# Kernel optimization log

Measured on AMD Instinct MI355X. Metric: run time of the kernel, lower is better.

## Reference

```python
import jax, jax.numpy as jnp
import numpy as np

B, T, IN_DIM, HIDDEN, OUT_DIM = 256, 4096, 2, 136, 68


def setup_inputs() -> dict:
    key = jax.random.key(0)
    ks = jax.random.split(key, 7)
    s_ih = 1.0 / np.sqrt(HIDDEN)
    return {
        "x": jax.random.normal(ks[0], (B, T, IN_DIM), dtype=jnp.float32),
        "W_ih": jax.random.uniform(ks[1], (HIDDEN, IN_DIM), jnp.float32, -s_ih, s_ih),
        "W_hh": jax.random.uniform(ks[2], (HIDDEN, HIDDEN), jnp.float32, -s_ih, s_ih),
        "b_ih": jax.random.uniform(ks[3], (HIDDEN,), jnp.float32, -s_ih, s_ih),
        "b_hh": jax.random.uniform(ks[4], (HIDDEN,), jnp.float32, -s_ih, s_ih),
        "W_fc": jax.random.uniform(ks[5], (OUT_DIM, HIDDEN), jnp.float32, -s_ih, s_ih),
        "b_fc": jax.random.uniform(ks[6], (OUT_DIM,), jnp.float32, -s_ih, s_ih),
    }


def reference(x, W_ih, W_hh, b_ih, b_hh, W_fc, b_fc):
    # Precompute input projection for all timesteps: [B, T, H]
    xp = jnp.einsum("bti,hi->bth", x, W_ih) + b_ih + b_hh
    h0 = jnp.zeros((x.shape[0], W_hh.shape[0]), dtype=x.dtype)

    def step(h, xp_t):  # h: [B,H], xp_t: [B,H]
        h_new = jnp.tanh(xp_t + h @ W_hh.T)
        return h_new, None

    # scan over time axis (move T to leading axis)
    h_last, _ = jax.lax.scan(step, h0, jnp.swapaxes(xp, 0, 1))
    # final linear head on last hidden state: [B, OUT]
    return h_last @ W_fc.T + b_fc
```

## Files before the change

kernel.cpp:

```cpp
#include <hip/hip_runtime.h>

#define BATCH 256
#define TSTEPS 4096
#define HID 136
#define HPADH 144
#define ODIM 68
#define THREADS 256

typedef _Float16 h2 __attribute__((ext_vector_type(2)));

#define BAR_LDS() asm volatile("s_waitcnt lgkmcnt(0)\n\ts_barrier" ::: "memory")

__device__ __forceinline__ float fast_tanh(float z) {
    float az = fabsf(z);
    float e = __expf(-2.0f * az);
    float r = (1.0f - e) * __builtin_amdgcn_rcpf(1.0f + e);
    return copysignf(r, z);
}

template <int CTRL>
__device__ __forceinline__ float dpp_add(float x) {
    int y = __builtin_amdgcn_update_dpp(0, __float_as_int(x), CTRL, 0xF, 0xF, false);
    return x + __int_as_float(y);
}
__device__ __forceinline__ float reduce8(float x) {
    x = dpp_add<0xB1>(x);
    x = dpp_add<0x4E>(x);
    x = dpp_add<0x141>(x);
    return x;
}

__device__ __forceinline__ h2 bc_h2(unsigned int u) {
    union { unsigned int u; h2 h; } c; c.u = u; return c.h;
}

#define RNN_STEP(HR, HW, XV)                                                   \
    {                                                                          \
        uint4 u0 = *(const uint4*)((HR) + 16 * ks);                            \
        uint4 u1 = *(const uint4*)((HR) + 16 * ks + 8);                        \
        unsigned int ut = *(const unsigned int*)((HR) + 128 + 2 * ks);         \
        h2 hq[9];                                                              \
        hq[0] = bc_h2(u0.x); hq[1] = bc_h2(u0.y);                              \
        hq[2] = bc_h2(u0.z); hq[3] = bc_h2(u0.w);                              \
        hq[4] = bc_h2(u1.x); hq[5] = bc_h2(u1.y);                              \
        hq[6] = bc_h2(u1.z); hq[7] = bc_h2(u1.w);                              \
        hq[8] = bc_h2(ut);                                                     \
        float a0 = 0.f, a1 = 0.f, a2 = 0.f, a3 = 0.f, a4 = 0.f;                \
        _Pragma("unroll")                                                      \
        for (int q = 0; q < 9; ++q) {                                          \
            a0 = __builtin_amdgcn_fdot2(hq[q], wq[0][q], a0, false);           \
            a1 = __builtin_amdgcn_fdot2(hq[q], wq[1][q], a1, false);           \
            a2 = __builtin_amdgcn_fdot2(hq[q], wq[2][q], a2, false);           \
            a3 = __builtin_amdgcn_fdot2(hq[q], wq[3][q], a3, false);           \
            a4 = __builtin_amdgcn_fdot2(hq[q], wq[4][q], a4, false);           \
        }                                                                      \
        a0 = reduce8(a0);                                                      \
        a1 = reduce8(a1);                                                      \
        a2 = reduce8(a2);                                                      \
        a3 = reduce8(a3);                                                      \
        a4 = reduce8(a4);                                                      \
        float s = a0;                                                          \
        s = (ks == 1) ? a1 : s;                                                \
        s = (ks == 2) ? a2 : s;                                                \
        s = (ks == 3) ? a3 : s;                                                \
        s = (ks == 4) ? a4 : s;                                                \
        float z = fmaf((XV).x, wih0, fmaf((XV).y, wih1, bias)) + s;            \
        float th = fast_tanh(z);                                               \
        if (ks < 4 || (ks == 4 && grp < 2)) (HW)[zrow] = (_Float16)th;         \
    }

__global__ __launch_bounds__(THREADS)
void rnn_fused_kernel(const float* __restrict__ x,
                      const float* __restrict__ W_ih,
                      const float* __restrict__ W_hh,
                      const float* __restrict__ b_ih,
                      const float* __restrict__ b_hh,
                      const float* __restrict__ W_fc,
                      const float* __restrict__ b_fc,
                      float* __restrict__ out)
{
    __shared__ __align__(16) _Float16 hA[HPADH];
    __shared__ __align__(16) _Float16 hB[HPADH];

    const int b   = blockIdx.x;
    const int tid = threadIdx.x;
    const int wv  = tid >> 6;
    const int grp = (tid >> 3) & 7;
    const int g   = tid >> 3;
    const int ks  = tid & 7;

    const int erow = 128 + 2 * wv + (g & 1);

    h2 wq[5][9];
#pragma unroll
    for (int j = 0; j < 5; ++j) {
        const int row = (j < 4) ? (4 * g + j) : erow;
#pragma unroll
        for (int q = 0; q < 9; ++q) {
            const int k = (q < 8) ? (16 * ks + 2 * q) : (128 + 2 * ks);
            const float v0 = (k     < HID) ? W_hh[row * HID + k]     : 0.0f;
            const float v1 = (k + 1 < HID) ? W_hh[row * HID + k + 1] : 0.0f;
            wq[j][q] = h2{(_Float16)v0, (_Float16)v1};
        }
    }
    const int zrow = (ks < 4) ? (4 * g + ks) : (ks == 4) ? erow : (4 * g);
    const float wih0 = W_ih[zrow * 2 + 0];
    const float wih1 = W_ih[zrow * 2 + 1];
    const float bias = b_ih[zrow] + b_hh[zrow];

    if (tid < HPADH) { hA[tid] = (_Float16)0.f; hB[tid] = (_Float16)0.f; }
    __syncthreads();

    const float2* xg = (const float2*)(x + (size_t)b * (TSTEPS * 2));
    float2 xc0 = xg[0], xc1 = xg[1];
    float2 xn0 = xg[2], xn1 = xg[3];

    for (int t = 0; t < TSTEPS; t += 2) {
        const int tf = (t + 4) & (TSTEPS - 1);
        const float2 xf0 = xg[tf];
        const float2 xf1 = xg[tf + 1];

        RNN_STEP(hA, hB, xc0);
        BAR_LDS();
        RNN_STEP(hB, hA, xc1);
        BAR_LDS();

        xc0 = xn0; xc1 = xn1;
        xn0 = xf0; xn1 = xf1;
    }

    if (tid < ODIM) {
        const int o = tid;
        float s = b_fc[o];
#pragma unroll 8
        for (int k = 0; k < HID; ++k)
            s = fmaf((float)hA[k], W_fc[o * HID + k], s);
        out[b * ODIM + o] = s;
    }
}

extern "C" void kernel_launch(void* const* d_in, const int* in_sizes, int n_in,
                              void* d_out, int out_size, void* d_ws, size_t ws_size,
                              hipStream_t stream) {
    const float* x    = (const float*)d_in[0];
    const float* W_ih = (const float*)d_in[1];
    const float* W_hh = (const float*)d_in[2];
    const float* b_ih = (const float*)d_in[3];
    const float* b_hh = (const float*)d_in[4];
    const float* W_fc = (const float*)d_in[5];
    const float* b_fc = (const float*)d_in[6];
    float* out = (float*)d_out;

    rnn_fused_kernel<<<BATCH, THREADS, 0, stream>>>(x, W_ih, W_hh, b_ih, b_hh,
                                                    W_fc, b_fc, out);
}
```

Before: 1.149 ms.

## Pack two batch rows per 512-thread block to interleave recurrences

Each block now runs two independent batch recurrences in separate halves of a 512-thread block, with per-half LDS hidden-state buffers, and launches half as many blocks. The intent is to let one CU overlap the latency chains of two sequences. In exchange, only half the CUs are used, and every step synchronizes 8 waves with a full __syncthreads instead of the lighter LDS-only barrier.

```diff
diff --git a/kernel.cpp b/kernel.cpp
--- a/kernel.cpp
+++ b/kernel.cpp
@@ -5,11 +5,10 @@
 #define HID 136
 #define HPADH 144
 #define ODIM 68
-#define THREADS 256
+#define THREADS 512
+#define NBLK (BATCH / 2)
 
 typedef _Float16 h2 __attribute__((ext_vector_type(2)));
-
-#define BAR_LDS() asm volatile("s_waitcnt lgkmcnt(0)\n\ts_barrier" ::: "memory")
 
 __device__ __forceinline__ float fast_tanh(float z) {
     float az = fabsf(z);
@@ -79,17 +78,19 @@
                       const float* __restrict__ b_fc,
                       float* __restrict__ out)
 {
-    __shared__ __align__(16) _Float16 hA[HPADH];
-    __shared__ __align__(16) _Float16 hB[HPADH];
+    __shared__ __align__(16) _Float16 hA[2][HPADH];
+    __shared__ __align__(16) _Float16 hB[2][HPADH];
 
-    const int b   = blockIdx.x;
     const int tid = threadIdx.x;
-    const int wv  = tid >> 6;
-    const int grp = (tid >> 3) & 7;
-    const int g   = tid >> 3;
+    const int sub = tid >> 8;
+    const int st  = tid & 255;
+    const int wvs = st >> 6;
+    const int grp = (st >> 3) & 7;
+    const int g   = st >> 3;
     const int ks  = tid & 7;
+    const int bb  = blockIdx.x * 2 + sub;
 
-    const int erow = 128 + 2 * wv + (g & 1);
+    const int erow = 128 + 2 * wvs + (g & 1);
 
     h2 wq[5][9];
 #pragma unroll
@@ -108,10 +109,13 @@
     const float wih1 = W_ih[zrow * 2 + 1];
     const float bias = b_ih[zrow] + b_hh[zrow];
 
-    if (tid < HPADH) { hA[tid] = (_Float16)0.f; hB[tid] = (_Float16)0.f; }
+    if (st < HPADH) { hA[sub][st] = (_Float16)0.f; hB[sub][st] = (_Float16)0.f; }
     __syncthreads();
 
-    const float2* xg = (const float2*)(x + (size_t)b * (TSTEPS * 2));
+    _Float16* const hAs = hA[sub];
+    _Float16* const hBs = hB[sub];
+
+    const float2* xg = (const float2*)(x + (size_t)bb * (TSTEPS * 2));
     float2 xc0 = xg[0], xc1 = xg[1];
     float2 xn0 = xg[2], xn1 = xg[3];
 
@@ -120,22 +124,22 @@
         const float2 xf0 = xg[tf];
         const float2 xf1 = xg[tf + 1];
 
-        RNN_STEP(hA, hB, xc0);
-        BAR_LDS();
-        RNN_STEP(hB, hA, xc1);
-        BAR_LDS();
+        RNN_STEP(hAs, hBs, xc0);
+        __syncthreads();
+        RNN_STEP(hBs, hAs, xc1);
+        __syncthreads();
 
         xc0 = xn0; xc1 = xn1;
         xn0 = xf0; xn1 = xf1;
     }
 
-    if (tid < ODIM) {
-        const int o = tid;
+    if (st < ODIM) {
+        const int o = st;
         float s = b_fc[o];
 #pragma unroll 8
         for (int k = 0; k < HID; ++k)
-            s = fmaf((float)hA[k], W_fc[o * HID + k], s);
-        out[b * ODIM + o] = s;
+            s = fmaf((float)hAs[k], W_fc[o * HID + k], s);
+        out[bb * ODIM + o] = s;
     }
 }
 
@@ -151,6 +155,6 @@
     const float* b_fc = (const float*)d_in[6];
     float* out = (float*)d_out;
 
-    rnn_fused_kernel<<<BATCH, THREADS, 0, stream>>>(x, W_ih, W_hh, b_ih, b_hh,
-                                                    W_fc, b_fc, out);
+    rnn_fused_kernel<<<NBLK, THREADS, 0, stream>>>(x, W_ih, W_hh, b_ih, b_hh,
+                                                   W_fc, b_fc, out);
 }
```

Result: slower. 1.772 ms (+54.2%).

## Assign one full hidden row per thread, dropping cross-lane DPP reduction

Applied to the files above, without the earlier changes.

Reworks the per-step matvec so each of 192 threads owns one full W_hh row (68 packed half2 weights in registers) and reads the whole hidden vector from LDS as broadcast loads. This removes the 8-lane DPP reduction, the select logic and the redundant row duplication, replacing them with a longer serial dot-product chain per thread. It uses 3 waves instead of 4, raises register pressure to roughly 68+68 VGPRs, and replaces the custom LDS barrier with __syncthreads.

```diff
diff --git a/kernel.cpp b/kernel.cpp
--- a/kernel.cpp
+++ b/kernel.cpp
@@ -3,13 +3,10 @@
 #define BATCH 256
 #define TSTEPS 4096
 #define HID 136
-#define HPADH 144
 #define ODIM 68
-#define THREADS 256
+#define THREADS 192
 
 typedef _Float16 h2 __attribute__((ext_vector_type(2)));
-
-#define BAR_LDS() asm volatile("s_waitcnt lgkmcnt(0)\n\ts_barrier" ::: "memory")
 
 __device__ __forceinline__ float fast_tanh(float z) {
     float az = fabsf(z);
@@ -18,55 +15,27 @@
     return copysignf(r, z);
 }
 
-template <int CTRL>
-__device__ __forceinline__ float dpp_add(float x) {
-    int y = __builtin_amdgcn_update_dpp(0, __float_as_int(x), CTRL, 0xF, 0xF, false);
-    return x + __int_as_float(y);
-}
-__device__ __forceinline__ float reduce8(float x) {
-    x = dpp_add<0xB1>(x);
-    x = dpp_add<0x4E>(x);
-    x = dpp_add<0x141>(x);
-    return x;
-}
-
 __device__ __forceinline__ h2 bc_h2(unsigned int u) {
     union { unsigned int u; h2 h; } c; c.u = u; return c.h;
 }
 
 #define RNN_STEP(HR, HW, XV)                                                   \
     {                                                                          \
-        uint4 u0 = *(const uint4*)((HR) + 16 * ks);                            \
-        uint4 u1 = *(const uint4*)((HR) + 16 * ks + 8);                        \
-        unsigned int ut = *(const unsigned int*)((HR) + 128 + 2 * ks);         \
-        h2 hq[9];                                                              \
-        hq[0] = bc_h2(u0.x); hq[1] = bc_h2(u0.y);                              \
-        hq[2] = bc_h2(u0.z); hq[3] = bc_h2(u0.w);                              \
-        hq[4] = bc_h2(u1.x); hq[5] = bc_h2(u1.y);                              \
-        hq[6] = bc_h2(u1.z); hq[7] = bc_h2(u1.w);                              \
-        hq[8] = bc_h2(ut);                                                     \
-        float a0 = 0.f, a1 = 0.f, a2 = 0.f, a3 = 0.f, a4 = 0.f;                \
+        uint4 hc[17];                                                          \
         _Pragma("unroll")                                                      \
-        for (int q = 0; q < 9; ++q) {                                          \
-            a0 = __builtin_amdgcn_fdot2(hq[q], wq[0][q], a0, false);           \
-            a1 = __builtin_amdgcn_fdot2(hq[q], wq[1][q], a1, false);           \
-            a2 = __builtin_amdgcn_fdot2(hq[q], wq[2][q], a2, false);           \
-            a3 = __builtin_amdgcn_fdot2(hq[q], wq[3][q], a3, false);           \
-            a4 = __builtin_amdgcn_fdot2(hq[q], wq[4][q], a4, false);           \
+        for (int i = 0; i < 17; ++i) hc[i] = ((const uint4*)(HR))[i];          \
+        float a0 = 0.f, a1 = 0.f, a2 = 0.f, a3 = 0.f;                          \
+        _Pragma("unroll")                                                      \
+        for (int i = 0; i < 17; ++i) {                                         \
+            a0 = __builtin_amdgcn_fdot2(bc_h2(hc[i].x), w[4 * i + 0], a0, false); \
+            a1 = __builtin_amdgcn_fdot2(bc_h2(hc[i].y), w[4 * i + 1], a1, false); \
+            a2 = __builtin_amdgcn_fdot2(bc_h2(hc[i].z), w[4 * i + 2], a2, false); \
+            a3 = __builtin_amdgcn_fdot2(bc_h2(hc[i].w), w[4 * i + 3], a3, false); \
         }                                                                      \
-        a0 = reduce8(a0);                                                      \
-        a1 = reduce8(a1);                                                      \
-        a2 = reduce8(a2);                                                      \
-        a3 = reduce8(a3);                                                      \
-        a4 = reduce8(a4);                                                      \
-        float s = a0;                                                          \
-        s = (ks == 1) ? a1 : s;                                                \
-        s = (ks == 2) ? a2 : s;                                                \
-        s = (ks == 3) ? a3 : s;                                                \
-        s = (ks == 4) ? a4 : s;                                                \
-        float z = fmaf((XV).x, wih0, fmaf((XV).y, wih1, bias)) + s;            \
+        float z = (a0 + a1) + (a2 + a3)                                        \
+                + fmaf((XV).x, wih0, fmaf((XV).y, wih1, bias));                \
         float th = fast_tanh(z);                                               \
-        if (ks < 4 || (ks == 4 && grp < 2)) (HW)[zrow] = (_Float16)th;         \
+        if (valid) (HW)[row] = (_Float16)th;                                   \
     }
 
 __global__ __launch_bounds__(THREADS)
@@ -79,36 +48,30 @@
                       const float* __restrict__ b_fc,
                       float* __restrict__ out)
 {
-    __shared__ __align__(16) _Float16 hA[HPADH];
-    __shared__ __align__(16) _Float16 hB[HPADH];
+    __shared__ __align__(16) _Float16 hA[HID];
+    __shared__ __align__(16) _Float16 hB[HID];
 
-    const int b   = blockIdx.x;
-    const int tid = threadIdx.x;
-    const int wv  = tid >> 6;
-    const int grp = (tid >> 3) & 7;
-    const int g   = tid >> 3;
-    const int ks  = tid & 7;
+    const int b     = blockIdx.x;
+    const int tid   = threadIdx.x;
+    const int row   = tid;
+    const bool valid = (row < HID);
+    const int rowc  = valid ? row : 0;
 
-    const int erow = 128 + 2 * wv + (g & 1);
+    h2 w[68];
+#pragma unroll
+    for (int p = 0; p < 68; ++p) {
+        const float v0 = valid ? W_hh[rowc * HID + 2 * p]     : 0.0f;
+        const float v1 = valid ? W_hh[rowc * HID + 2 * p + 1] : 0.0f;
+        w[p] = h2{(_Float16)v0, (_Float16)v1};
+    }
+    const float wih0 = valid ? W_ih[rowc * 2 + 0] : 0.0f;
+    const float wih1 = valid ? W_ih[rowc * 2 + 1] : 0.0f;
+    const float bias = valid ? (b_ih[rowc] + b_hh[rowc]) : 0.0f;
 
-    h2 wq[5][9];
-#pragma unroll
-    for (int j = 0; j < 5; ++j) {
-        const int row = (j < 4) ? (4 * g + j) : erow;
-#pragma unroll
-        for (int q = 0; q < 9; ++q) {
-            const int k = (q < 8) ? (16 * ks + 2 * q) : (128 + 2 * ks);
-            const float v0 = (k     < HID) ? W_hh[row * HID + k]     : 0.0f;
-            const float v1 = (k + 1 < HID) ? W_hh[row * HID + k + 1] : 0.0f;
-            wq[j][q] = h2{(_Float16)v0, (_Float16)v1};
-        }
+    if (tid < HID / 2) {
+        ((unsigned int*)hA)[tid] = 0u;
+        ((unsigned int*)hB)[tid] = 0u;
     }
-    const int zrow = (ks < 4) ? (4 * g + ks) : (ks == 4) ? erow : (4 * g);
-    const float wih0 = W_ih[zrow * 2 + 0];
-    const float wih1 = W_ih[zrow * 2 + 1];
-    const float bias = b_ih[zrow] + b_hh[zrow];
-
-    if (tid < HPADH) { hA[tid] = (_Float16)0.f; hB[tid] = (_Float16)0.f; }
     __syncthreads();
 
     const float2* xg = (const float2*)(x + (size_t)b * (TSTEPS * 2));
@@ -121,9 +84,9 @@
         const float2 xf1 = xg[tf + 1];
 
         RNN_STEP(hA, hB, xc0);
-        BAR_LDS();
+        __syncthreads();
         RNN_STEP(hB, hA, xc1);
-        BAR_LDS();
+        __syncthreads();
 
         xc0 = xn0; xc1 = xn1;
         xn0 = xf0; xn1 = xf1;
```

After: 1.423 ms. 1.24x slower.
